# Kernel optimization log

Hardware: AMD Instinct MI355X
Metric: run time of the kernel (lower is better)

The kernel has to match this reference:

```python
import jax, jax.numpy as jnp
import numpy as np

EPS = 1e-8


def setup_inputs() -> dict:
    key = jax.random.key(0)
    k1, k2 = jax.random.split(key)
    latent = jax.random.normal(k1, (16, 192, 64, 64), dtype=jnp.float32)
    codebook = jax.random.normal(k2, (1024, 192), dtype=jnp.float32)
    # codebook rows are unit-normalized at init in the original module
    codebook = codebook / jnp.linalg.norm(codebook, axis=-1, keepdims=True)
    return {"latent": latent, "codebook": codebook}


def reference(latent, codebook):
    b, c, h, w = latent.shape
    # [B,C,H,W] -> [N, C]
    x = jnp.transpose(latent, (0, 2, 3, 1)).reshape(-1, c)
    x = x / (jnp.linalg.norm(x, axis=-1, keepdims=True) + EPS)
    x2 = jnp.sum(x * x, axis=-1, keepdims=True)            # [N,1]
    c2 = jnp.sum(codebook * codebook, axis=-1)             # [K]
    dist_sq = x2 - 2.0 * jnp.einsum('nd,kd->nk', x, codebook) + c2[None, :]
    indices = jnp.argmin(dist_sq, axis=-1)                 # [N]
    quantized_flat = codebook[indices]                     # [N,C] gather
    quantized = jnp.transpose(quantized_flat.reshape(b, h, w, c), (0, 3, 1, 2))
    return quantized, indices.reshape(b, h, w)
```

## Files before the change

### kernel.cpp

```cpp
#include <hip/hip_runtime.h>
#include <hip/hip_bf16.h>


#define NPTS   65536
#define DIMS   192
#define KCB    1024
#define HW     4096
#define QELEMS 12582912

typedef __attribute__((ext_vector_type(8))) _Float16 f16x8;
typedef __attribute__((ext_vector_type(4))) _Float16 f16x4;
typedef __attribute__((ext_vector_type(4))) float f32x4;

#define MARGIN_Q 4864u

__device__ __forceinline__ void async_load16(const void* g, void* l) {
    __builtin_amdgcn_global_load_lds(
        (const __attribute__((address_space(1))) unsigned int*)g,
        (__attribute__((address_space(3))) unsigned int*)l, 16, 0, 0);
}

__device__ __forceinline__ unsigned qdist(float d) {
    float t = (d + 1.0f) * 1048576.0f;
    t = fminf(fmaxf(t, 0.0f), 4194303.0f);
    return (unsigned)t;
}

__device__ __forceinline__ void top2_merge(unsigned& b, unsigned& s,
                                           unsigned ob, unsigned os) {
    unsigned nb = min(b, ob);
    unsigned ns = min(max(b, ob), min(s, os));
    b = nb; s = ns;
}

__global__ __launch_bounds__(256) void k_prep_cb16(const float* __restrict__ cbk,
                                                   _Float16* __restrict__ Bpf) {
    int id = blockIdx.x * 256 + threadIdx.x;
    if (id >= KCB * DIMS) return;
    int k = id / DIMS, d = id % DIMS;
    Bpf[((size_t)(d >> 6) * KCB + k) * 64 + (d & 63)] = (_Float16)cbk[id];
}

__global__ __launch_bounds__(256) void k_c2(const float* __restrict__ cbk,
                                            float* __restrict__ c2) {
    int k = blockIdx.x * 256 + threadIdx.x;
    if (k >= KCB) return;
    const float4* row = (const float4*)(cbk + (size_t)k * DIMS);
    float s = 0.f;
    #pragma unroll
    for (int i = 0; i < DIMS / 4; ++i) {
        float4 v = row[i];
        s += v.x * v.x + v.y * v.y + v.z * v.z + v.w * v.w;
    }
    c2[k] = s;
}

__global__ __launch_bounds__(256) void k_cbT(const float* __restrict__ cbk,
                                             float* __restrict__ cbkT) {
    __shared__ float q[64 * 193];
    const int tid = threadIdx.x;
    const int k0 = blockIdx.x * 64;
    const int lane = tid & 63;
    const int grp = tid >> 6;
    for (int r = grp; r < 64; r += 4) {
        const float* row = cbk + (size_t)(k0 + r) * DIMS;
        for (int c = lane; c < DIMS; c += 64) q[r * 193 + c] = row[c];
    }
    __syncthreads();
    for (int d = grp; d < DIMS; d += 4) {
        cbkT[(size_t)d * KCB + k0 + lane] = q[lane * 193 + d];
    }
}

__global__ __launch_bounds__(256, 2) void k_gemm_f(const float* __restrict__ latent,
                                                   const _Float16* __restrict__ Bpf,
                                                   const float* __restrict__ c2,
                                                   const float* __restrict__ cbk,
                                                   float* __restrict__ out_q,
                                                   float* __restrict__ idxf,
                                                   int* __restrict__ list,
                                                   int* __restrict__ cnt) {
    __shared__ __align__(16) _Float16 As[128 * 200];
    __shared__ __align__(16) _Float16 Bs[128 * 64];
    __shared__ float inv_s[128];
    __shared__ uint2 t2buf[256];
    __shared__ int sidx[128];

    const int tid = threadIdx.x;
    const int wave = tid >> 6;
    const int lane = tid & 63;
    const int quad = lane >> 4;
    const int l15 = lane & 15;
    const int wm = (wave >> 1) * 64;
    const int wn = (wave & 1) * 64;
    const int n0 = blockIdx.x * 128;
    const int bB = n0 >> 12;
    const int hw0 = n0 & 4095;

    {
        float* part = (float*)Bs;
        const float* lat = latent + (size_t)bB * DIMS * HW + hw0;
        const int p = tid & 127, ch = tid >> 7;
        float ss = 0.f;
        #pragma unroll 4
        for (int i = 0; i < 24; ++i) {
            int c0 = i * 8 + ch * 4;
            float v0 = lat[(size_t)(c0 + 0) * HW + p];
            float v1 = lat[(size_t)(c0 + 1) * HW + p];
            float v2 = lat[(size_t)(c0 + 2) * HW + p];
            float v3 = lat[(size_t)(c0 + 3) * HW + p];
            ss = fmaf(v0, v0, fmaf(v1, v1, fmaf(v2, v2, fmaf(v3, v3, ss))));
            f16x4 h = { (_Float16)v0, (_Float16)v1, (_Float16)v2, (_Float16)v3 };
            *(f16x4*)&As[p * 200 + c0] = h;
        }
        part[ch * 128 + p] = ss;
        __syncthreads();
        if (tid < 128)
            inv_s[tid] = 1.0f / (sqrtf(part[tid] + part[128 + tid]) + 1e-8f);
        __syncthreads();
    }

    unsigned rb[16], rs[16];
    #pragma unroll
    for (int i = 0; i < 16; ++i) { rb[i] = 0xFFFFFFFFu; rs[i] = 0xFFFFFFFFu; }

    for (int nb = 0; nb < 8; ++nb) {
        f32x4 acc[4][4];
        #pragma unroll
        for (int mt = 0; mt < 4; ++mt)
            #pragma unroll
            for (int nt = 0; nt < 4; ++nt)
                #pragma unroll
                for (int r = 0; r < 4; ++r) acc[mt][nt][r] = 0.f;

        for (int g = 0; g < 3; ++g) {
            __syncthreads();
            #pragma unroll
            for (int i = 0; i < 4; ++i) {
                int u = i * 256 + tid;
                int m = u >> 3, c = u & 7;
                int sw = c ^ (m & 7);
                async_load16(Bpf + (((size_t)g * KCB + nb * 128 + m) * 8 + sw) * 8,
                             &Bs[u * 8]);
            }
            __syncthreads();
            #pragma unroll
            for (int s = 0; s < 2; ++s) {
                f16x8 af[4], bfr[4];
                #pragma unroll
                for (int mt = 0; mt < 4; ++mt) {
                    int m = wm + mt * 16 + l15;
                    af[mt] = *(const f16x8*)&As[m * 200 + g * 64 + s * 32 + quad * 8];
                }
                #pragma unroll
                for (int nt = 0; nt < 4; ++nt) {
                    int n = wn + nt * 16 + l15;
                    int c = (s * 4 + quad) ^ (n & 7);
                    bfr[nt] = *(const f16x8*)&Bs[n * 64 + c * 8];
                }
                #pragma unroll
                for (int mt = 0; mt < 4; ++mt)
                    #pragma unroll
                    for (int nt = 0; nt < 4; ++nt)
                        acc[mt][nt] = __builtin_amdgcn_mfma_f32_16x16x32_f16(
                            af[mt], bfr[nt], acc[mt][nt], 0, 0, 0);
            }
        }

        int kbase = nb * 128 + wn;
        float c2v[4];
        #pragma unroll
        for (int nt = 0; nt < 4; ++nt) c2v[nt] = c2[kbase + nt * 16 + l15];
        #pragma unroll
        for (int mt = 0; mt < 4; ++mt) {
            #pragma unroll
            for (int r = 0; r < 4; ++r) {
                float inv = inv_s[wm + mt * 16 + quad * 4 + r];
                unsigned p[4];
                #pragma unroll
                for (int nt = 0; nt < 4; ++nt) {
                    float dist = fmaf(-2.f * inv, acc[mt][nt][r], c2v[nt]);
                    p[nt] = (qdist(dist) << 10) | (unsigned)(kbase + nt * 16 + l15);
                }
                unsigned b01 = min(p[0], p[1]), s01 = max(p[0], p[1]);
                unsigned b23 = min(p[2], p[3]), s23 = max(p[2], p[3]);
                unsigned nbb = min(b01, b23);
                unsigned nbs = min(max(b01, b23), min(s01, s23));
                top2_merge(rb[mt * 4 + r], rs[mt * 4 + r], nbb, nbs);
            }
        }
    }

    __syncthreads();
    #pragma unroll
    for (int i = 0; i < 16; ++i) {
        unsigned b = rb[i], s = rs[i];
        #pragma unroll
        for (int off = 1; off < 16; off <<= 1) {
            unsigned ob = __shfl_xor(b, off, 64);
            unsigned os = __shfl_xor(s, off, 64);
            top2_merge(b, s, ob, os);
        }
        if (l15 == 0) {
            int mt = i >> 2, r = i & 3;
            int mloc = wm + mt * 16 + quad * 4 + r;
            t2buf[mloc * 2 + (wave & 1)] = make_uint2(b, s);
        }
    }
    __syncthreads();
    if (tid < 128) {
        uint2 x = t2buf[tid * 2];
        uint2 y = t2buf[tid * 2 + 1];
        unsigned b = x.x, s = x.y;
        top2_merge(b, s, y.x, y.y);
        int k = (int)(b & 1023u);
        sidx[tid] = k;
        idxf[n0 + tid] = (float)k;
        if (((s >> 10) - (b >> 10)) < MARGIN_Q) {
            int pos = atomicAdd(cnt, 1);
            list[pos] = n0 + tid;
        }
    }
    __syncthreads();

    float* q = (float*)As;
    for (int chk = 0; chk < 4; ++chk) {
        int p0 = chk * 32;
        for (int r = wave; r < 32; r += 4) {
            const float* row = cbk + (size_t)sidx[p0 + r] * DIMS;
            for (int c = lane; c < DIMS; c += 64) q[r * 193 + c] = row[c];
        }
        __syncthreads();
        float* ob = out_q + (size_t)bB * DIMS * HW + hw0 + p0;
        #pragma unroll
        for (int i = 0; i < 24; ++i) {
            int u = i * 256 + tid;
            int c = u >> 5, p = u & 31;
            ob[(size_t)c * HW + p] = q[p * 193 + c];
        }
        __syncthreads();
    }
}

__global__ __launch_bounds__(256) void k_rescore16(const float* __restrict__ latent,
                                                   const float* __restrict__ cbkT,
                                                   const float* __restrict__ cbk,
                                                   const float* __restrict__ c2,
                                                   const int* __restrict__ list,
                                                   const int* __restrict__ cnt,
                                                   float* __restrict__ out_q,
                                                   float* __restrict__ idxf) {
    __shared__ float xs[16][200];
    __shared__ float part[16][16];
    __shared__ float inv_s[16];
    __shared__ unsigned long long best[16];
    const int tid = threadIdx.x;
    const int count = *cnt;
    const float4* ct = (const float4*)cbkT;
    const int j = tid >> 4, dl = tid & 15;

    for (int base = blockIdx.x * 16; base < count; base += gridDim.x * 16) {
        __syncthreads();
        float ss = 0.f;
        int n = 0, bb = 0, hw = 0;
        bool valid = (base + j) < count;
        if (valid) {
            n = list[base + j]; bb = n >> 12; hw = n & 4095;
            #pragma unroll
            for (int i = 0; i < 12; ++i) {
                int d = dl + i * 16;
                float v = latent[((size_t)bb * DIMS + d) * HW + hw];
                xs[j][d] = v;
                ss = fmaf(v, v, ss);
            }
        }
        part[j][dl] = ss;
        if (tid < 16) best[tid] = ~0ull;
        __syncthreads();
        if (tid < 16) {
            float s = 0.f;
            #pragma unroll
            for (int i = 0; i < 16; ++i) s += part[tid][i];
            inv_s[tid] = 1.0f / (sqrtf(s) + 1e-8f);
        }
        __syncthreads();

        float4 a[16];
        #pragma unroll
        for (int p = 0; p < 16; ++p) a[p] = make_float4(0.f, 0.f, 0.f, 0.f);
        for (int d = 0; d < DIMS; d += 4) {
            float4 cv0 = ct[(size_t)(d + 0) * 256 + tid];
            float4 cv1 = ct[(size_t)(d + 1) * 256 + tid];
            float4 cv2 = ct[(size_t)(d + 2) * 256 + tid];
            float4 cv3 = ct[(size_t)(d + 3) * 256 + tid];
            #pragma unroll
            for (int p = 0; p < 16; ++p) {
                float4 xv = *(const float4*)&xs[p][d];
                a[p].x = fmaf(xv.x, cv0.x, a[p].x); a[p].y = fmaf(xv.x, cv0.y, a[p].y);
                a[p].z = fmaf(xv.x, cv0.z, a[p].z); a[p].w = fmaf(xv.x, cv0.w, a[p].w);
                a[p].x = fmaf(xv.y, cv1.x, a[p].x); a[p].y = fmaf(xv.y, cv1.y, a[p].y);
                a[p].z = fmaf(xv.y, cv1.z, a[p].z); a[p].w = fmaf(xv.y, cv1.w, a[p].w);
                a[p].x = fmaf(xv.z, cv2.x, a[p].x); a[p].y = fmaf(xv.z, cv2.y, a[p].y);
                a[p].z = fmaf(xv.z, cv2.z, a[p].z); a[p].w = fmaf(xv.z, cv2.w, a[p].w);
                a[p].x = fmaf(xv.w, cv3.x, a[p].x); a[p].y = fmaf(xv.w, cv3.y, a[p].y);
                a[p].z = fmaf(xv.w, cv3.z, a[p].z); a[p].w = fmaf(xv.w, cv3.w, a[p].w);
            }
        }
        #pragma unroll
        for (int p = 0; p < 16; ++p) {
            float inv = inv_s[p];
            float dot4[4] = {a[p].x, a[p].y, a[p].z, a[p].w};
            unsigned long long loc = ~0ull;
            #pragma unroll
            for (int e = 0; e < 4; ++e) {
                int k = 4 * tid + e;
                float dist = c2[k] - 2.f * inv * dot4[e];
                unsigned ub = __float_as_uint(dist);
                ub ^= (ub >> 31) ? 0xFFFFFFFFu : 0x80000000u;
                unsigned long long pk =
                    ((unsigned long long)ub << 32) | (unsigned)k;
                loc = loc < pk ? loc : pk;
            }
            #pragma unroll
            for (int off = 1; off < 64; off <<= 1) {
                unsigned long long o = __shfl_xor(loc, off, 64);
                loc = loc < o ? loc : o;
            }
            if ((tid & 63) == 0) atomicMin(&best[p], loc);
        }
        __syncthreads();
        if (valid) {
            int kk = (int)(best[j] & 0xFFFFFFFFull);
            #pragma unroll
            for (int i = 0; i < 12; ++i) {
                int d = dl + i * 16;
                out_q[((size_t)bb * DIMS + d) * HW + hw] = cbk[(size_t)kk * DIMS + d];
            }
            if (dl == 0) idxf[n] = (float)kk;
        }
    }
}

__global__ __launch_bounds__(256) void k_norms_fb(const float* __restrict__ latent,
                                                  float* __restrict__ inv_norm) {
    __shared__ float red[256];
    const int tid = threadIdx.x;
    const int n0 = blockIdx.x * 128;
    const int nl = tid & 127;
    const int half = tid >> 7;
    const int b = n0 >> 12;
    const int hw = (n0 & 4095) + nl;
    const float* base = latent + (size_t)b * DIMS * HW + hw;
    float ssq = 0.f;
    for (int c = half; c < DIMS; c += 2) {
        float v = base[(size_t)c * HW];
        ssq = fmaf(v, v, ssq);
    }
    red[tid] = ssq;
    __syncthreads();
    if (half == 0) {
        float s = red[tid] + red[tid + 128];
        inv_norm[n0 + nl] = 1.0f / (sqrtf(s) + 1e-8f);
    }
}

#define LDX  132
__global__ __launch_bounds__(256) void k_dist_fb(const float* __restrict__ latent,
                                                 const float* __restrict__ cbk,
                                                 const float* __restrict__ inv_norm,
                                                 const float* __restrict__ c2,
                                                 int* __restrict__ idx_out,
                                                 float* __restrict__ idxf_out) {
    __shared__ __align__(16) float xsm[64 * LDX];
    __shared__ __align__(16) float csm[64 * LDX];
    __shared__ unsigned long long red[128];
    const int tid = threadIdx.x;
    const int n0 = blockIdx.x * 128;
    const int b = n0 >> 12;
    const int hw0 = n0 & 4095;
    const int kt = tid & 15;
    const int mt = tid >> 4;
    const float* lat_base = latent + (size_t)b * DIMS * HW + hw0;
    float inv[8];
    #pragma unroll
    for (int i = 0; i < 8; ++i) inv[i] = inv_norm[n0 + mt * 8 + i];
    float best[8];
    int bidx[8];
    #pragma unroll
    for (int i = 0; i < 8; ++i) { best[i] = 3.4e38f; bidx[i] = 0; }
    const int nl = tid & 127;
    const int cp = tid >> 7;
    for (int k0 = 0; k0 < KCB; k0 += 128) {
        float acc[8][8];
        #pragma unroll
        for (int i = 0; i < 8; ++i)
            #pragma unroll
            for (int j = 0; j < 8; ++j) acc[i][j] = 0.f;
        for (int d0 = 0; d0 < DIMS; d0 += 64) {
            __syncthreads();
            for (int cc = cp; cc < 64; cc += 2)
                xsm[cc * LDX + nl] = lat_base[(size_t)(d0 + cc) * HW + nl];
            #pragma unroll
            for (int i = 0; i < 8; ++i) {
                int f4 = tid + 256 * i;
                int kk = f4 >> 4;
                int dq = f4 & 15;
                float4 v = *(const float4*)(cbk + (size_t)(k0 + kk) * DIMS + d0 + dq * 4);
                csm[(dq * 4 + 0) * LDX + kk] = v.x;
                csm[(dq * 4 + 1) * LDX + kk] = v.y;
                csm[(dq * 4 + 2) * LDX + kk] = v.z;
                csm[(dq * 4 + 3) * LDX + kk] = v.w;
            }
            __syncthreads();
            for (int d = 0; d < 64; ++d) {
                const float* xr = &xsm[d * LDX + mt * 8];
                const float* cr = &csm[d * LDX + kt * 8];
                float x8[8], c8[8];
                *(float4*)&x8[0] = *(const float4*)&xr[0];
                *(float4*)&x8[4] = *(const float4*)&xr[4];
                *(float4*)&c8[0] = *(const float4*)&cr[0];
                *(float4*)&c8[4] = *(const float4*)&cr[4];
                #pragma unroll
                for (int i = 0; i < 8; ++i)
                    #pragma unroll
                    for (int j = 0; j < 8; ++j)
                        acc[i][j] = fmaf(x8[i], c8[j], acc[i][j]);
            }
        }
        float cc2[8];
        #pragma unroll
        for (int j = 0; j < 8; ++j) cc2[j] = c2[k0 + kt * 8 + j];
        #pragma unroll
        for (int i = 0; i < 8; ++i)
            #pragma unroll
            for (int j = 0; j < 8; ++j) {
                float t = inv[i] * acc[i][j];
                float dist = fmaf(-2.f, t, cc2[j]);
                int kidx = k0 + kt * 8 + j;
                if (dist < best[i]) { best[i] = dist; bidx[i] = kidx; }
            }
    }
    if (tid < 128) red[tid] = ~0ull;
    __syncthreads();
    #pragma unroll
    for (int i = 0; i < 8; ++i) {
        unsigned long long p =
            ((unsigned long long)__float_as_uint(best[i]) << 32) | (unsigned)bidx[i];
        atomicMin(&red[mt * 8 + i], p);
    }
    __syncthreads();
    if (tid < 128) {
        int k = (int)(red[tid] & 0xFFFFFFFFu);
        idx_out[n0 + tid] = k;
        idxf_out[n0 + tid] = (float)k;
    }
}

__global__ __launch_bounds__(256) void k_gather(const float* __restrict__ cbk,
                                                const int* __restrict__ idx,
                                                float* __restrict__ out) {
    __shared__ float q[64 * 193];
    __shared__ int sidx[64];
    const int tid = threadIdx.x;
    const int n0 = blockIdx.x * 64;
    const int b = n0 >> 12;
    const int hw0 = n0 & 4095;
    const int lane = tid & 63;
    const int grp = tid >> 6;

    if (tid < 64) sidx[tid] = idx[n0 + tid];
    __syncthreads();
    for (int r = grp; r < 64; r += 4) {
        const float* row = cbk + (size_t)sidx[r] * DIMS;
        for (int c = lane; c < DIMS; c += 64) q[r * 193 + c] = row[c];
    }
    __syncthreads();
    float* obase = out + (size_t)b * DIMS * HW + hw0;
    for (int c = grp; c < DIMS; c += 4) {
        obase[(size_t)c * HW + lane] = q[lane * 193 + c];
    }
}

extern "C" void kernel_launch(void* const* d_in, const int* in_sizes, int n_in,
                              void* d_out, int out_size, void* d_ws, size_t ws_size,
                              hipStream_t stream) {
    const float* latent = (const float*)d_in[0];
    const float* cbk = (const float*)d_in[1];
    float* out = (float*)d_out;
    float* out_q = out;
    float* out_idx = out + QELEMS;

    if (ws_size >= 2u * 1024u * 1024u) {
        char* w = (char*)d_ws;
        _Float16* Bpf = (_Float16*)w;
        float* cbkT = (float*)(w + 393216);
        float* c2 = (float*)(w + 1179648);
        int* list = (int*)(w + 1183744);
        int* cnt = (int*)(w + 1445888);

        hipMemsetAsync(cnt, 0, 4, stream);
        k_prep_cb16<<<768, 256, 0, stream>>>(cbk, Bpf);
        k_c2<<<4, 256, 0, stream>>>(cbk, c2);
        k_cbT<<<KCB / 64, 256, 0, stream>>>(cbk, cbkT);
        k_gemm_f<<<512, 256, 0, stream>>>(latent, Bpf, c2, cbk, out_q, out_idx,
                                          list, cnt);
        k_rescore16<<<512, 256, 0, stream>>>(latent, cbkT, cbk, c2, list, cnt,
                                             out_q, out_idx);
    } else {
        float* inv_norm = (float*)d_ws;
        float* c2 = inv_norm + NPTS;
        int* idx = (int*)(c2 + KCB);
        k_norms_fb<<<NPTS / 128, 256, 0, stream>>>(latent, inv_norm);
        k_c2<<<4, 256, 0, stream>>>(cbk, c2);
        k_dist_fb<<<NPTS / 128, 256, 0, stream>>>(latent, cbk, inv_norm, c2, idx, out_idx);
        k_gather<<<NPTS / 64, 256, 0, stream>>>(cbk, idx, out_q);
    }
}
```

Baseline: 234.6 us.

## Track top-3 candidates and rescore ambiguous points cheaply before full fallback

The GEMM kernel now keeps the top-3 candidates per point, packed as truncated float distance plus index, and writes them to workspace. A new fix kernel recomputes exact fp32 distances only for those three candidates. Points whose third candidate is also close go to a smaller full-rescore kernel. The codebook prep kernels are merged into one, and B fragments are read straight from global memory instead of being staged through LDS. This aims to shrink the expensive full rescore work and the LDS staging syncs, at the cost of an extra launch, a larger workspace, and uncached global B reads.

```diff
diff --git a/kernel.cpp b/kernel.cpp
--- a/kernel.cpp
+++ b/kernel.cpp
@@ -12,51 +12,19 @@
 typedef __attribute__((ext_vector_type(4))) _Float16 f16x4;
 typedef __attribute__((ext_vector_type(4))) float f32x4;
 
-#define MARGIN_Q 4864u
-
-__device__ __forceinline__ void async_load16(const void* g, void* l) {
-    __builtin_amdgcn_global_load_lds(
-        (const __attribute__((address_space(1))) unsigned int*)g,
-        (__attribute__((address_space(3))) unsigned int*)l, 16, 0, 0);
-}
-
-__device__ __forceinline__ unsigned qdist(float d) {
-    float t = (d + 1.0f) * 1048576.0f;
-    t = fminf(fmaxf(t, 0.0f), 4194303.0f);
-    return (unsigned)t;
-}
-
-__device__ __forceinline__ void top2_merge(unsigned& b, unsigned& s,
-                                           unsigned ob, unsigned os) {
-    unsigned nb = min(b, ob);
-    unsigned ns = min(max(b, ob), min(s, os));
-    b = nb; s = ns;
-}
-
-__global__ __launch_bounds__(256) void k_prep_cb16(const float* __restrict__ cbk,
-                                                   _Float16* __restrict__ Bpf) {
-    int id = blockIdx.x * 256 + threadIdx.x;
-    if (id >= KCB * DIMS) return;
-    int k = id / DIMS, d = id % DIMS;
-    Bpf[((size_t)(d >> 6) * KCB + k) * 64 + (d & 63)] = (_Float16)cbk[id];
-}
-
-__global__ __launch_bounds__(256) void k_c2(const float* __restrict__ cbk,
-                                            float* __restrict__ c2) {
-    int k = blockIdx.x * 256 + threadIdx.x;
-    if (k >= KCB) return;
-    const float4* row = (const float4*)(cbk + (size_t)k * DIMS);
-    float s = 0.f;
-    #pragma unroll
-    for (int i = 0; i < DIMS / 4; ++i) {
-        float4 v = row[i];
-        s += v.x * v.x + v.y * v.y + v.z * v.z + v.w * v.w;
-    }
-    c2[k] = s;
-}
-
-__global__ __launch_bounds__(256) void k_cbT(const float* __restrict__ cbk,
-                                             float* __restrict__ cbkT) {
+#define MVAL 6.0e-3f
+
+__device__ __forceinline__ void ins3(unsigned& a, unsigned& b, unsigned& c,
+                                     unsigned v) {
+    unsigned m1 = max(a, v); a = min(a, v);
+    unsigned m2 = max(b, m1); b = min(b, m1);
+    c = min(c, m2);
+}
+
+__global__ __launch_bounds__(256) void k_prep(const float* __restrict__ cbk,
+                                              _Float16* __restrict__ Bpf,
+                                              float* __restrict__ c2,
+                                              float* __restrict__ cbkT) {
     __shared__ float q[64 * 193];
     const int tid = threadIdx.x;
     const int k0 = blockIdx.x * 64;
@@ -67,23 +35,37 @@
         for (int c = lane; c < DIMS; c += 64) q[r * 193 + c] = row[c];
     }
     __syncthreads();
-    for (int d = grp; d < DIMS; d += 4) {
+    if (tid < 64) {
+        float s = 0.f;
+        for (int c = 0; c < DIMS; ++c) { float v = q[tid * 193 + c]; s = fmaf(v, v, s); }
+        c2[k0 + tid] = s;
+    }
+    #pragma unroll
+    for (int i = 0; i < 12; ++i) {
+        int u = i * 256 + tid;
+        int kk = u / 48, c4 = u % 48, d0 = c4 * 4;
+        f16x4 h = { (_Float16)q[kk * 193 + d0], (_Float16)q[kk * 193 + d0 + 1],
+                    (_Float16)q[kk * 193 + d0 + 2], (_Float16)q[kk * 193 + d0 + 3] };
+        *(f16x4*)&Bpf[((size_t)(d0 >> 6) * KCB + k0 + kk) * 64 + (d0 & 63)] = h;
+    }
+    for (int d = grp; d < DIMS; d += 4)
         cbkT[(size_t)d * KCB + k0 + lane] = q[lane * 193 + d];
-    }
-}
-
-__global__ __launch_bounds__(256, 2) void k_gemm_f(const float* __restrict__ latent,
-                                                   const _Float16* __restrict__ Bpf,
-                                                   const float* __restrict__ c2,
-                                                   const float* __restrict__ cbk,
-                                                   float* __restrict__ out_q,
-                                                   float* __restrict__ idxf,
-                                                   int* __restrict__ list,
-                                                   int* __restrict__ cnt) {
-    __shared__ __align__(16) _Float16 As[128 * 200];
-    __shared__ __align__(16) _Float16 Bs[128 * 64];
+}
+
+__global__ __launch_bounds__(256, 2) void k_gemm_f2(const float* __restrict__ latent,
+                                                    const _Float16* __restrict__ Bpf,
+                                                    const float* __restrict__ c2,
+                                                    const float* __restrict__ cbk,
+                                                    float* __restrict__ out_q,
+                                                    float* __restrict__ idxf,
+                                                    float* __restrict__ inv_g,
+                                                    ushort4* __restrict__ cand4,
+                                                    int* __restrict__ list,
+                                                    int* __restrict__ cnt) {
+    __shared__ __align__(16) char smem[51200];
+    _Float16* As = (_Float16*)smem;
+    __shared__ float part[256];
     __shared__ float inv_s[128];
-    __shared__ uint2 t2buf[256];
     __shared__ int sidx[128];
 
     const int tid = threadIdx.x;
@@ -98,7 +80,6 @@
     const int hw0 = n0 & 4095;
 
     {
-        float* part = (float*)Bs;
         const float* lat = latent + (size_t)bB * DIMS * HW + hw0;
         const int p = tid & 127, ch = tid >> 7;
         float ss = 0.f;
@@ -115,14 +96,24 @@
         }
         part[ch * 128 + p] = ss;
         __syncthreads();
-        if (tid < 128)
-            inv_s[tid] = 1.0f / (sqrtf(part[tid] + part[128 + tid]) + 1e-8f);
-        __syncthreads();
-    }
-
-    unsigned rb[16], rs[16];
-    #pragma unroll
-    for (int i = 0; i < 16; ++i) { rb[i] = 0xFFFFFFFFu; rs[i] = 0xFFFFFFFFu; }
+        if (tid < 128) {
+            float iv = 1.0f / (sqrtf(part[tid] + part[128 + tid]) + 1e-8f);
+            inv_s[tid] = iv;
+            inv_g[n0 + tid] = iv;
+        }
+        __syncthreads();
+    }
+
+    float minv[16];
+    #pragma unroll
+    for (int mt = 0; mt < 4; ++mt)
+        #pragma unroll
+        for (int r = 0; r < 4; ++r)
+            minv[mt * 4 + r] = -2.0f * inv_s[wm + mt * 16 + quad * 4 + r];
+
+    unsigned ra[16], rbv[16], rc[16];
+    #pragma unroll
+    for (int i = 0; i < 16; ++i) { ra[i] = ~0u; rbv[i] = ~0u; rc[i] = ~0u; }
 
     for (int nb = 0; nb < 8; ++nb) {
         f32x4 acc[4][4];
@@ -133,17 +124,8 @@
                 #pragma unroll
                 for (int r = 0; r < 4; ++r) acc[mt][nt][r] = 0.f;
 
+        #pragma unroll
         for (int g = 0; g < 3; ++g) {
-            __syncthreads();
-            #pragma unroll
-            for (int i = 0; i < 4; ++i) {
-                int u = i * 256 + tid;
-                int m = u >> 3, c = u & 7;
-                int sw = c ^ (m & 7);
-                async_load16(Bpf + (((size_t)g * KCB + nb * 128 + m) * 8 + sw) * 8,
-                             &Bs[u * 8]);
-            }
-            __syncthreads();
             #pragma unroll
             for (int s = 0; s < 2; ++s) {
                 f16x8 af[4], bfr[4];
@@ -154,9 +136,9 @@
                 }
                 #pragma unroll
                 for (int nt = 0; nt < 4; ++nt) {
-                    int n = wn + nt * 16 + l15;
-                    int c = (s * 4 + quad) ^ (n & 7);
-                    bfr[nt] = *(const f16x8*)&Bs[n * 64 + c * 8];
+                    int n = nb * 128 + wn + nt * 16 + l15;
+                    bfr[nt] = *(const f16x8*)&Bpf[((size_t)g * KCB + n) * 64
+                                                  + s * 32 + quad * 8];
                 }
                 #pragma unroll
                 for (int mt = 0; mt < 4; ++mt)
@@ -168,62 +150,73 @@
         }
 
         int kbase = nb * 128 + wn;
-        float c2v[4];
-        #pragma unroll
-        for (int nt = 0; nt < 4; ++nt) c2v[nt] = c2[kbase + nt * 16 + l15];
+        float c2p[4];
+        unsigned kc[4];
+        #pragma unroll
+        for (int nt = 0; nt < 4; ++nt) {
+            kc[nt] = (unsigned)(kbase + nt * 16 + l15);
+            c2p[nt] = c2[kc[nt]] + 1.0f;
+        }
         #pragma unroll
         for (int mt = 0; mt < 4; ++mt) {
             #pragma unroll
             for (int r = 0; r < 4; ++r) {
-                float inv = inv_s[wm + mt * 16 + quad * 4 + r];
-                unsigned p[4];
+                int i = mt * 4 + r;
+                float mi = minv[i];
                 #pragma unroll
                 for (int nt = 0; nt < 4; ++nt) {
-                    float dist = fmaf(-2.f * inv, acc[mt][nt][r], c2v[nt]);
-                    p[nt] = (qdist(dist) << 10) | (unsigned)(kbase + nt * 16 + l15);
+                    float d1 = fmaf(mi, acc[mt][nt][r], c2p[nt]);
+                    unsigned u = (__float_as_uint(d1) & 0xFFFFFC00u) | kc[nt];
+                    ins3(ra[i], rbv[i], rc[i], u);
                 }
-                unsigned b01 = min(p[0], p[1]), s01 = max(p[0], p[1]);
-                unsigned b23 = min(p[2], p[3]), s23 = max(p[2], p[3]);
-                unsigned nbb = min(b01, b23);
-                unsigned nbs = min(max(b01, b23), min(s01, s23));
-                top2_merge(rb[mt * 4 + r], rs[mt * 4 + r], nbb, nbs);
-            }
-        }
-    }
-
-    __syncthreads();
+            }
+        }
+    }
+
     #pragma unroll
     for (int i = 0; i < 16; ++i) {
-        unsigned b = rb[i], s = rs[i];
+        unsigned a = ra[i], b = rbv[i], c = rc[i];
         #pragma unroll
         for (int off = 1; off < 16; off <<= 1) {
+            unsigned oa = __shfl_xor(a, off, 64);
             unsigned ob = __shfl_xor(b, off, 64);
-            unsigned os = __shfl_xor(s, off, 64);
-            top2_merge(b, s, ob, os);
-        }
+            unsigned oc = __shfl_xor(c, off, 64);
+            ins3(a, b, c, oa); ins3(a, b, c, ob); ins3(a, b, c, oc);
+        }
+        ra[i] = a; rbv[i] = b; rc[i] = c;
+    }
+    __syncthreads();
+    unsigned* t3 = (unsigned*)smem;
+    #pragma unroll
+    for (int i = 0; i < 16; ++i) {
         if (l15 == 0) {
             int mt = i >> 2, r = i & 3;
-            int mloc = wm + mt * 16 + quad * 4 + r;
-            t2buf[mloc * 2 + (wave & 1)] = make_uint2(b, s);
+            int m = wm + mt * 16 + quad * 4 + r;
+            t3[(m * 2 + (wave & 1)) * 3 + 0] = ra[i];
+            t3[(m * 2 + (wave & 1)) * 3 + 1] = rbv[i];
+            t3[(m * 2 + (wave & 1)) * 3 + 2] = rc[i];
         }
     }
     __syncthreads();
     if (tid < 128) {
-        uint2 x = t2buf[tid * 2];
-        uint2 y = t2buf[tid * 2 + 1];
-        unsigned b = x.x, s = x.y;
-        top2_merge(b, s, y.x, y.y);
-        int k = (int)(b & 1023u);
-        sidx[tid] = k;
-        idxf[n0 + tid] = (float)k;
-        if (((s >> 10) - (b >> 10)) < MARGIN_Q) {
-            int pos = atomicAdd(cnt, 1);
-            list[pos] = n0 + tid;
-        }
-    }
-    __syncthreads();
-
-    float* q = (float*)As;
+        unsigned a = t3[(tid * 2) * 3], b = t3[(tid * 2) * 3 + 1], c = t3[(tid * 2) * 3 + 2];
+        ins3(a, b, c, t3[(tid * 2 + 1) * 3 + 0]);
+        ins3(a, b, c, t3[(tid * 2 + 1) * 3 + 1]);
+        ins3(a, b, c, t3[(tid * 2 + 1) * 3 + 2]);
+        int k1 = (int)(a & 1023u);
+        sidx[tid] = k1;
+        idxf[n0 + tid] = (float)k1;
+        float d1v = __uint_as_float(a & 0xFFFFFC00u);
+        float d2v = __uint_as_float(b & 0xFFFFFC00u);
+        float d3v = __uint_as_float(c & 0xFFFFFC00u);
+        unsigned fl = ((d2v - d1v) < MVAL ? 1u : 0u) | ((d3v - d1v) < MVAL ? 2u : 0u);
+        cand4[n0 + tid] = make_ushort4((ushort)k1, (ushort)(b & 1023u),
+                                       (ushort)(c & 1023u), (ushort)fl);
+        if (fl & 2u) { int pos = atomicAdd(cnt, 1); list[pos] = n0 + tid; }
+    }
+    __syncthreads();
+
+    float* q = (float*)smem;
     for (int chk = 0; chk < 4; ++chk) {
         int p0 = chk * 32;
         for (int r = wave; r < 32; r += 4) {
@@ -242,14 +235,96 @@
     }
 }
 
-__global__ __launch_bounds__(256) void k_rescore16(const float* __restrict__ latent,
-                                                   const float* __restrict__ cbkT,
-                                                   const float* __restrict__ cbk,
-                                                   const float* __restrict__ c2,
-                                                   const int* __restrict__ list,
-                                                   const int* __restrict__ cnt,
-                                                   float* __restrict__ out_q,
-                                                   float* __restrict__ idxf) {
+__global__ __launch_bounds__(256) void k_fix(const float* __restrict__ latent,
+                                             const float* __restrict__ cbk,
+                                             const float* __restrict__ c2,
+                                             const float* __restrict__ inv_g,
+                                             const ushort4* __restrict__ cand4,
+                                             float* __restrict__ out_q,
+                                             float* __restrict__ idxf) {
+    __shared__ float xs[64 * 193];
+    __shared__ ushort4 scand[64];
+    __shared__ float pd[64][3];
+    __shared__ int plist[64];
+    __shared__ int fcnt;
+    const int tid = threadIdx.x;
+
+    for (int h = 0; h < 2; ++h) {
+        const int base = blockIdx.x * 128 + h * 64;
+        __syncthreads();
+        if (tid == 0) fcnt = 0;
+        __syncthreads();
+        if (tid < 64) {
+            ushort4 cc = cand4[base + tid];
+            scand[tid] = cc;
+            if (cc.w & 1) { int pos = atomicAdd(&fcnt, 1); plist[pos] = tid; }
+        }
+        __syncthreads();
+        const int F = fcnt;
+        if (F == 0) continue;
+
+        const int bB = base >> 12, hw0 = base & 4095;
+        const float* lat = latent + (size_t)bB * DIMS * HW + hw0;
+        const int p = tid & 63, c4 = tid >> 6;
+        for (int i = 0; i < 48; ++i) {
+            int c = c4 + i * 4;
+            xs[p * 193 + c] = lat[(size_t)c * HW + p];
+        }
+        __syncthreads();
+
+        if (tid < 3 * F) {
+            int i = tid / 3, cd = tid - 3 * i;
+            int pt = plist[i];
+            ushort4 cc = scand[pt];
+            int k = (cd == 0) ? cc.x : ((cd == 1) ? cc.y : cc.z);
+            const float4* crow = (const float4*)(cbk + (size_t)k * DIMS);
+            float dot = 0.f;
+            #pragma unroll 8
+            for (int d4 = 0; d4 < 48; ++d4) {
+                float4 cv = crow[d4];
+                const float* xr = &xs[pt * 193 + d4 * 4];
+                dot = fmaf(xr[0], cv.x, dot);
+                dot = fmaf(xr[1], cv.y, dot);
+                dot = fmaf(xr[2], cv.z, dot);
+                dot = fmaf(xr[3], cv.w, dot);
+            }
+            pd[pt][cd] = c2[k] - 2.f * inv_g[base + pt] * dot;
+        }
+        __syncthreads();
+        if (tid < F) {
+            int pt = plist[tid];
+            ushort4 cc = scand[pt];
+            int k[3] = { cc.x, cc.y, cc.z };
+            float d[3] = { pd[pt][0], pd[pt][1], pd[pt][2] };
+            if (k[1] < k[0]) { int tk = k[0]; k[0] = k[1]; k[1] = tk;
+                               float td = d[0]; d[0] = d[1]; d[1] = td; }
+            if (k[2] < k[1]) { int tk = k[1]; k[1] = k[2]; k[2] = tk;
+                               float td = d[1]; d[1] = d[2]; d[2] = td; }
+            if (k[1] < k[0]) { int tk = k[0]; k[0] = k[1]; k[1] = tk;
+                               float td = d[0]; d[0] = d[1]; d[1] = td; }
+            int bk = k[0]; float bd = d[0];
+            if (d[1] < bd) { bd = d[1]; bk = k[1]; }
+            if (d[2] < bd) { bd = d[2]; bk = k[2]; }
+            if (bk != (int)cc.x) {
+                int n = base + pt;
+                idxf[n] = (float)bk;
+                const float* row = cbk + (size_t)bk * DIMS;
+                float* oq = out_q + (size_t)bB * DIMS * HW + hw0 + pt;
+                for (int dd = 0; dd < DIMS; ++dd)
+                    oq[(size_t)dd * HW] = row[dd];
+            }
+        }
+    }
+}
+
+__global__ __launch_bounds__(256) void k_full(const float* __restrict__ latent,
+                                              const float* __restrict__ cbkT,
+                                              const float* __restrict__ cbk,
+                                              const float* __restrict__ c2,
+                                              const int* __restrict__ list,
+                                              const int* __restrict__ cnt,
+                                              float* __restrict__ out_q,
+                                              float* __restrict__ idxf) {
     __shared__ float xs[16][200];
     __shared__ float part[16][16];
     __shared__ float inv_s[16];
@@ -288,28 +363,22 @@
         float4 a[16];
         #pragma unroll
         for (int p = 0; p < 16; ++p) a[p] = make_float4(0.f, 0.f, 0.f, 0.f);
-        for (int d = 0; d < DIMS; d += 4) {
+        for (int d = 0; d < DIMS; d += 2) {
             float4 cv0 = ct[(size_t)(d + 0) * 256 + tid];
             float4 cv1 = ct[(size_t)(d + 1) * 256 + tid];
-            float4 cv2 = ct[(size_t)(d + 2) * 256 + tid];
-            float4 cv3 = ct[(size_t)(d + 3) * 256 + tid];
             #pragma unroll
             for (int p = 0; p < 16; ++p) {
-                float4 xv = *(const float4*)&xs[p][d];
-                a[p].x = fmaf(xv.x, cv0.x, a[p].x); a[p].y = fmaf(xv.x, cv0.y, a[p].y);
-                a[p].z = fmaf(xv.x, cv0.z, a[p].z); a[p].w = fmaf(xv.x, cv0.w, a[p].w);
-                a[p].x = fmaf(xv.y, cv1.x, a[p].x); a[p].y = fmaf(xv.y, cv1.y, a[p].y);
-                a[p].z = fmaf(xv.y, cv1.z, a[p].z); a[p].w = fmaf(xv.y, cv1.w, a[p].w);
-                a[p].x = fmaf(xv.z, cv2.x, a[p].x); a[p].y = fmaf(xv.z, cv2.y, a[p].y);
-                a[p].z = fmaf(xv.z, cv2.z, a[p].z); a[p].w = fmaf(xv.z, cv2.w, a[p].w);
-                a[p].x = fmaf(xv.w, cv3.x, a[p].x); a[p].y = fmaf(xv.w, cv3.y, a[p].y);
-                a[p].z = fmaf(xv.w, cv3.z, a[p].z); a[p].w = fmaf(xv.w, cv3.w, a[p].w);
+                float x0 = xs[p][d], x1 = xs[p][d + 1];
+                a[p].x = fmaf(x0, cv0.x, a[p].x); a[p].y = fmaf(x0, cv0.y, a[p].y);
+                a[p].z = fmaf(x0, cv0.z, a[p].z); a[p].w = fmaf(x0, cv0.w, a[p].w);
+                a[p].x = fmaf(x1, cv1.x, a[p].x); a[p].y = fmaf(x1, cv1.y, a[p].y);
+                a[p].z = fmaf(x1, cv1.z, a[p].z); a[p].w = fmaf(x1, cv1.w, a[p].w);
             }
         }
         #pragma unroll
         for (int p = 0; p < 16; ++p) {
             float inv = inv_s[p];
-            float dot4[4] = {a[p].x, a[p].y, a[p].z, a[p].w};
+            float dot4[4] = { a[p].x, a[p].y, a[p].z, a[p].w };
             unsigned long long loc = ~0ull;
             #pragma unroll
             for (int e = 0; e < 4; ++e) {
@@ -317,8 +386,7 @@
                 float dist = c2[k] - 2.f * inv * dot4[e];
                 unsigned ub = __float_as_uint(dist);
                 ub ^= (ub >> 31) ? 0xFFFFFFFFu : 0x80000000u;
-                unsigned long long pk =
-                    ((unsigned long long)ub << 32) | (unsigned)k;
+                unsigned long long pk = ((unsigned long long)ub << 32) | (unsigned)k;
                 loc = loc < pk ? loc : pk;
             }
             #pragma unroll
@@ -339,6 +407,20 @@
             if (dl == 0) idxf[n] = (float)kk;
         }
     }
+}
+
+__global__ __launch_bounds__(256) void k_c2(const float* __restrict__ cbk,
+                                            float* __restrict__ c2) {
+    int k = blockIdx.x * 256 + threadIdx.x;
+    if (k >= KCB) return;
+    const float4* row = (const float4*)(cbk + (size_t)k * DIMS);
+    float s = 0.f;
+    #pragma unroll
+    for (int i = 0; i < DIMS / 4; ++i) {
+        float4 v = row[i];
+        s += v.x * v.x + v.y * v.y + v.z * v.z + v.w * v.w;
+    }
+    c2[k] = s;
 }
 
 __global__ __launch_bounds__(256) void k_norms_fb(const float* __restrict__ latent,
@@ -490,22 +572,24 @@
     float* out_q = out;
     float* out_idx = out + QELEMS;
 
-    if (ws_size >= 2u * 1024u * 1024u) {
+    if (ws_size >= 3u * 1024u * 1024u) {
         char* w = (char*)d_ws;
         _Float16* Bpf = (_Float16*)w;
         float* cbkT = (float*)(w + 393216);
         float* c2 = (float*)(w + 1179648);
-        int* list = (int*)(w + 1183744);
-        int* cnt = (int*)(w + 1445888);
+        float* inv_g = (float*)(w + 1183744);
+        ushort4* cand4 = (ushort4*)(w + 1445888);
+        int* list = (int*)(w + 1970176);
+        int* cnt = (int*)(w + 2232320);
 
         hipMemsetAsync(cnt, 0, 4, stream);
-        k_prep_cb16<<<768, 256, 0, stream>>>(cbk, Bpf);
-        k_c2<<<4, 256, 0, stream>>>(cbk, c2);
-        k_cbT<<<KCB / 64, 256, 0, stream>>>(cbk, cbkT);
-        k_gemm_f<<<512, 256, 0, stream>>>(latent, Bpf, c2, cbk, out_q, out_idx,
-                                          list, cnt);
-        k_rescore16<<<512, 256, 0, stream>>>(latent, cbkT, cbk, c2, list, cnt,
-                                             out_q, out_idx);
+        k_prep<<<KCB / 64, 256, 0, stream>>>(cbk, Bpf, c2, cbkT);
+        k_gemm_f2<<<512, 256, 0, stream>>>(latent, Bpf, c2, cbk, out_q, out_idx,
+                                           inv_g, cand4, list, cnt);
+        k_fix<<<512, 256, 0, stream>>>(latent, cbk, c2, inv_g, cand4,
+                                       out_q, out_idx);
+        k_full<<<64, 256, 0, stream>>>(latent, cbkT, cbk, c2, list, cnt,
+                                       out_q, out_idx);
     } else {
         float* inv_norm = (float*)d_ws;
         float* c2 = inv_norm + NPTS;
```

Measured after the change: 341.1 us. 1.45x slower.
